# Optimization experiments

Hardware: AMD Instinct MI355X
Metric: run time of the kernel (lower is better)

The kernel has to match this reference:

```python
import jax, jax.numpy as jnp
import numpy as np

N = 20000      # nodes
E = 320000     # edges
B = 128        # graphs in batch
DIN = 64       # in_channels == out_channels (residual)
DEDGE = 64     # edge_attr_dim
DINS = 64      # ins_dim
H = 2          # heads
C = 64         # out_channels per head
L = 2          # num_ins (conv layers)
SLOPE = 0.2    # leaky relu negative slope
EPS = 1e-5     # batchnorm eps


def setup_inputs() -> dict:
    key = jax.random.key(0)
    ks = jax.random.split(key, 12)
    s = 0.05  # small glorot-ish init scale
    return {
        "x": jax.random.normal(ks[0], (N, DIN), jnp.float32),
        "edge_index": jax.random.randint(ks[1], (2, E), 0, N),
        "edge_attr": jax.random.normal(ks[2], (E, DEDGE), jnp.float32),
        "instr_vectors": jax.random.normal(ks[3], (L, B, DINS), jnp.float32),
        "batch": jnp.sort(jax.random.randint(ks[4], (N,), 0, B)),
        "W_l": jax.random.normal(ks[5], (L, DIN + DINS, H * C), jnp.float32) * s,
        "W_e": jax.random.normal(ks[6], (L, DEDGE + DINS, H * C), jnp.float32) * s,
        "att_l": jax.random.normal(ks[7], (L, H, C), jnp.float32) * s,
        "att_r": jax.random.normal(ks[8], (L, H, C), jnp.float32) * s,
        "att_e": jax.random.normal(ks[9], (L, H, C), jnp.float32) * s,
        "bias": jnp.zeros((L, C), jnp.float32),
        "bn_gamma": jnp.ones((L - 1, C), jnp.float32),
        "bn_beta": jnp.zeros((L - 1, C), jnp.float32),
    }


def reference(x, edge_index, edge_attr, instr_vectors, batch,
              W_l, W_e, att_l, att_r, att_e, bias, bn_gamma, bn_beta):
    src, dst = edge_index[0], edge_index[1]  # j -> i (source_to_target)
    h = x
    for i in range(L):
        ins = instr_vectors[i]                                   # [B, DINS]
        x_cat = jnp.concatenate([h, ins[batch]], axis=-1)        # [N, DIN+DINS]
        e_cat = jnp.concatenate([edge_attr, ins[batch[src]]], axis=-1)  # [E, ...]
        xl = (x_cat @ W_l[i]).reshape(-1, H, C)                  # [N,H,C] (lin_l == lin_r)
        al = (xl * att_l[i]).sum(-1)                             # [N,H]
        ar = (xl * att_r[i]).sum(-1)                             # [N,H]
        eh = (e_cat @ W_e[i]).reshape(-1, H, C)                  # [E,H,C]
        ae = (eh * att_e[i]).sum(-1)                             # [E,H]
        a = al[src] + ar[dst] + ae                               # [E,H]
        a = jnp.where(a > 0, a, SLOPE * a)                       # leaky relu
        # segment softmax over incoming edges of each target node
        m = jax.ops.segment_max(a, dst, num_segments=N)          # [N,H]
        ex = jnp.exp(a - m[dst])
        ssum = jax.ops.segment_sum(ex, dst, num_segments=N)
        alpha = ex / (ssum[dst] + 1e-16)                         # [E,H]
        out = jax.ops.segment_sum(xl[src] * alpha[:, :, None], dst, num_segments=N)
        out = out.mean(axis=1) + bias[i]                         # concat=False -> head mean
        h = out + h                                              # residual
        if i != L - 1:
            mu = h.mean(axis=0)
            var = ((h - mu) ** 2).mean(axis=0)                   # biased var (BN training)
            h = (h - mu) / jnp.sqrt(var + EPS) * bn_gamma[i] + bn_beta[i]
            h = jax.nn.relu(h)
    return h
```

## Files before the change

kernel.cpp:

```cpp
#include <hip/hip_runtime.h>
#include <hip/hip_fp16.h>
#include <math.h>

#define NN 20000
#define NE 320000
#define NB 128
#define SLOPE 0.2f
#define BN_EPS 1e-5f
#define NBLK 79
#define ROWS 65

__device__ __forceinline__ unsigned short f2bf(float f) {
    unsigned int u = __float_as_uint(f);
    unsigned int r = (u + 0x7FFFu + ((u >> 16) & 1u)) >> 16;
    return (unsigned short)r;
}
__device__ __forceinline__ float bf2f(unsigned short h) {
    return __uint_as_float(((unsigned int)h) << 16);
}

__global__ __launch_bounds__(256) void k_hist(const int* __restrict__ dst, int* __restrict__ deg) {
    int e = blockIdx.x * 256 + threadIdx.x;
    if (e < NE) atomicAdd(&deg[dst[e]], 1);
}

__global__ __launch_bounds__(256) void k_scanA(const int* __restrict__ deg, int* __restrict__ bsum) {
    __shared__ int wsum[4];
    int t = threadIdx.x;
    int idx = blockIdx.x * 256 + t;
    int v = (idx < NN) ? deg[idx] : 0;
    for (int off = 32; off > 0; off >>= 1) v += __shfl_xor(v, off);
    if ((t & 63) == 0) wsum[t >> 6] = v;
    __syncthreads();
    if (t == 0) bsum[blockIdx.x] = wsum[0] + wsum[1] + wsum[2] + wsum[3];
}

__global__ __launch_bounds__(64) void k_scanB(const int* __restrict__ bsum, int* __restrict__ boff,
                                              int* __restrict__ rowptr) {
    int l = threadIdx.x;
    int v0 = (l < NBLK) ? bsum[l] : 0;
    int v1 = (64 + l < NBLK) ? bsum[64 + l] : 0;
    int o0 = v0, o1 = v1;
    for (int off = 1; off < 64; off <<= 1) { int u = __shfl_up(v0, off); if (l >= off) v0 += u; }
    int tot0 = __shfl(v0, 63);
    for (int off = 1; off < 64; off <<= 1) { int u = __shfl_up(v1, off); if (l >= off) v1 += u; }
    int tot1 = __shfl(v1, 63);
    if (l < NBLK) boff[l] = v0 - o0;
    if (64 + l < NBLK) boff[64 + l] = tot0 + v1 - o1;
    if (l == 0) rowptr[NN] = tot0 + tot1;
}

__global__ __launch_bounds__(256) void k_scanC(const int* __restrict__ deg, const int* __restrict__ boff,
                                               int* __restrict__ rowptr, int* __restrict__ cursor) {
    __shared__ int wsum[4];
    int t = threadIdx.x, lane = t & 63, w = t >> 6;
    int idx = blockIdx.x * 256 + t;
    int v = (idx < NN) ? deg[idx] : 0;
    int incl = v;
    for (int off = 1; off < 64; off <<= 1) { int u = __shfl_up(incl, off); if (lane >= off) incl += u; }
    if (lane == 63) wsum[w] = incl;
    __syncthreads();
    int pre = 0;
    for (int i = 0; i < w; ++i) pre += wsum[i];
    int excl = incl - v + pre + boff[blockIdx.x];
    if (idx < NN) { rowptr[idx] = excl; cursor[idx] = excl; }
}

__global__ __launch_bounds__(256) void k_p1(const float* __restrict__ We, const float* __restrict__ atte,
                                            float* __restrict__ ve01, float* __restrict__ w2e01) {
    int L = blockIdx.x;
    const float* WeL = We + (size_t)L * 128 * 128;
    const float* aeL = atte + L * 128;
    int t = threadIdx.x;
    int h = (t >> 6) & 1;
    int k = t & 63;
    int row = (t < 128) ? k : (64 + k);
    float acc = 0.f;
    for (int c = 0; c < 64; ++c) acc += WeL[row * 128 + h * 64 + c] * aeL[h * 64 + c];
    if (t < 128) ve01[L * 128 + t] = acc;
    else        w2e01[L * 128 + (t - 128)] = acc;
}

__global__ __launch_bounds__(256) void k_p2both(const float* __restrict__ instr, const float* __restrict__ Wl,
                                                const float* __restrict__ w2e01,
                                                float* __restrict__ insl01, float* __restrict__ ce01) {
    int blk = blockIdx.x, t = threadIdx.x;
    if (blk < 128) {
        int L = blk >> 6;
        int idx = (blk & 63) * 256 + t;
        int b = idx >> 7, j = idx & 127;
        const float* ins = instr + (size_t)L * NB * 64;
        const float* WlL = Wl + (size_t)L * 128 * 128;
        float acc = 0.f;
        for (int k = 0; k < 64; ++k) acc += ins[b * 64 + k] * WlL[(64 + k) * 128 + j];
        insl01[(size_t)L * 16384 + idx] = acc;
    } else {
        int L = blk - 128;
        int b = t >> 1, h = t & 1;
        const float* ins = instr + (size_t)L * NB * 64;
        const float* w2 = w2e01 + L * 128 + h * 64;
        float acc = 0.f;
        for (int k = 0; k < 64; ++k) acc += ins[b * 64 + k] * w2[k];
        ce01[L * 256 + b * 2 + h] = acc;
    }
}

__global__ __launch_bounds__(256) void k_node(const float* __restrict__ hcur, const float* __restrict__ Wl,
                                              const float* __restrict__ insl, const int* __restrict__ batch,
                                              const float* __restrict__ attl, const float* __restrict__ attr_,
                                              const float2* __restrict__ ce2,
                                              const float* __restrict__ scsh, int use_bn,
                                              unsigned short* __restrict__ xlh,
                                              float* __restrict__ alc, float* __restrict__ ar) {
    __shared__ float sh[8 * 64];
    int t = threadIdx.x;
    int row0 = blockIdx.x * 8;
    for (int idx = t; idx < 512; idx += 256) {
        int r = idx >> 6, k = idx & 63;
        int n = row0 + r;
        float hv = (n < NN) ? hcur[n * 64 + k] : 0.f;
        if (use_bn) hv = fmaxf(hv * scsh[k] + scsh[64 + k], 0.f);
        sh[idx] = hv;
    }
    __syncthreads();
    int w = t >> 6, lane = t & 63;
    int h = w & 1;
    int rbase = (w >> 1) * 4;
    int j = h * 64 + lane;
    float attlv = attl[j];
    float attrv = attr_[j];
    float acc0 = 0.f, acc1 = 0.f, acc2 = 0.f, acc3 = 0.f;
    for (int k = 0; k < 64; ++k) {
        float wv = Wl[k * 128 + j];
        acc0 += sh[(rbase + 0) * 64 + k] * wv;
        acc1 += sh[(rbase + 1) * 64 + k] * wv;
        acc2 += sh[(rbase + 2) * 64 + k] * wv;
        acc3 += sh[(rbase + 3) * 64 + k] * wv;
    }
    float accs[4] = {acc0, acc1, acc2, acc3};
    for (int rr = 0; rr < 4; ++rr) {
        int n = row0 + rbase + rr;
        if (n >= NN) break;
        int b = batch[n];
        float v = accs[rr] + insl[b * 128 + j];
        xlh[(size_t)n * 128 + j] = f2bf(v);
        float pl = v * attlv, pr = v * attrv;
        for (int off = 32; off > 0; off >>= 1) {
            pl += __shfl_xor(pl, off);
            pr += __shfl_xor(pr, off);
        }
        if (lane == 0) {
            float2 cb = ce2[b];
            alc[n * 2 + h] = pl + (h ? cb.y : cb.x);
            ar[n * 2 + h] = pr;
        }
    }
}

__global__ __launch_bounds__(64) void k_sced(const int* __restrict__ src, const int* __restrict__ dst,
                                             const float* __restrict__ eattr, const float* __restrict__ ve01,
                                             const float2* __restrict__ alc2, const float2* __restrict__ ar2,
                                             int* __restrict__ cursor, int4* __restrict__ einfo) {
    __shared__ float se[64 * ROWS];
    __shared__ float svT[256];
    int lane = threadIdx.x;
#pragma unroll
    for (int i = 0; i < 4; ++i) {
        int idx = i * 64 + lane;
        svT[idx] = ve01[(idx & 3) * 64 + (idx >> 2)];
    }
    int ebase = blockIdx.x * 64;
    const float4* gsrc = (const float4*)eattr + (size_t)ebase * 16;
#pragma unroll
    for (int i = 0; i < 16; ++i) {
        int fi = i * 64 + lane;
        float4 f = gsrc[fi];
        int el = fi >> 4, q = fi & 15;
        float* dp = se + el * ROWS + q * 4;
        dp[0] = f.x; dp[1] = f.y; dp[2] = f.z; dp[3] = f.w;
    }
    const float* row = se + lane * ROWS;
    float d0 = 0.f, d1 = 0.f, d2 = 0.f, d3 = 0.f;
#pragma unroll
    for (int k = 0; k < 64; ++k) {
        float fv = row[k];
        float4 vt = *(const float4*)&svT[4 * k];
        d0 += fv * vt.x; d1 += fv * vt.y; d2 += fv * vt.z; d3 += fv * vt.w;
    }
    int e = ebase + lane;
    int s = src[e], dd = dst[e];
    float2 al = alc2[s], arr = ar2[dd];
    float a0 = al.x + arr.x + d0;
    float a1 = al.y + arr.y + d1;
    a0 = (a0 > 0.f) ? a0 : SLOPE * a0;
    a1 = (a1 > 0.f) ? a1 : SLOPE * a1;
    __half2 ex = __floats2half2_rn(__expf(a0), __expf(a1));
    __half2 d23 = __floats2half2_rn(d2, d3);
    int pos = atomicAdd(&cursor[dd], 1);
    einfo[pos] = make_int4(s | (dd << 15), *(int*)&d23, s, *(int*)&ex);
}

__global__ __launch_bounds__(256) void k_attnexp(const int4* __restrict__ einfo,
                                                 const float2* __restrict__ alc2, const float2* __restrict__ ar2,
                                                 int2* __restrict__ rec1) {
    int p = blockIdx.x * 256 + threadIdx.x;
    if (p >= NE) return;
    int4 r = einfo[p];
    int s = r.x & 0x7FFF, d = r.x >> 15;
    __half2 hd = *(__half2*)&r.y;
    float2 dv = __half22float2(hd);
    float2 a_l = alc2[s];
    float2 a_r = ar2[d];
    float a0 = a_l.x + a_r.x + dv.x;
    float a1 = a_l.y + a_r.y + dv.y;
    a0 = (a0 > 0.f) ? a0 : SLOPE * a0;
    a1 = (a1 > 0.f) ? a1 : SLOPE * a1;
    __half2 hx = __floats2half2_rn(__expf(a0), __expf(a1));
    rec1[p] = make_int2(s, *(int*)&hx);
}

__global__ __launch_bounds__(256) void k_gather(const int* __restrict__ rowptr, const int2* __restrict__ rec,
                                                int stride,
                                                const unsigned int* __restrict__ xl32,
                                                const float* __restrict__ bias, const float* __restrict__ hprev,
                                                const float* __restrict__ scsh, int use_bn,
                                                float* __restrict__ hnew) {
    int t = threadIdx.x;
    int w = t >> 6, lane = t & 63;
    int n = blockIdx.x * 4 + w;
    if (n >= NN) return;
    int r0 = rowptr[n], r1 = rowptr[n + 1];
    float acc0 = 0.f, acc1 = 0.f, ss = 0.f;
    const unsigned int* xlp = xl32 + lane;
#pragma unroll 8
    for (int p = r0; p < r1; ++p) {
        int2 r = rec[(size_t)p * stride];
        __half2 hx = *(__half2*)&r.y;
        float2 e2 = __half22float2(hx);
        float ex = (lane < 32) ? e2.x : e2.y;
        unsigned int pr = xlp[(size_t)r.x * 64];
        ss += ex;
        acc0 += ex * bf2f((unsigned short)(pr & 0xFFFFu));
        acc1 += ex * bf2f((unsigned short)(pr >> 16));
    }
    float inv_s = 1.f / (ss + 1e-16f);
    acc0 *= inv_s; acc1 *= inv_s;
    float o0 = 0.5f * (acc0 + __shfl_xor(acc0, 32));
    float o1 = 0.5f * (acc1 + __shfl_xor(acc1, 32));
    if (lane < 32) {
        float2 hv = ((const float2*)(hprev + (size_t)n * 64))[lane];
        if (use_bn) {
            float2 sc = ((const float2*)scsh)[lane];
            float2 sf = ((const float2*)(scsh + 64))[lane];
            hv.x = fmaxf(hv.x * sc.x + sf.x, 0.f);
            hv.y = fmaxf(hv.y * sc.y + sf.y, 0.f);
        }
        float2 bv = ((const float2*)bias)[lane];
        float2 o;
        o.x = o0 + bv.x + hv.x;
        o.y = o1 + bv.y + hv.y;
        ((float2*)(hnew + (size_t)n * 64))[lane] = o;
    }
}

__global__ __launch_bounds__(256) void k_bnstat(const float* __restrict__ hbuf,
                                                float* __restrict__ part, float* __restrict__ partsq) {
    __shared__ float sA[256], sB[256];
    int t = threadIdx.x;
    int c = t & 63, r = t >> 6;
    int n0 = blockIdx.x * 80;
    float s = 0.f, s2 = 0.f;
    for (int i = 0; i < 20; ++i) {
        float v = hbuf[(size_t)(n0 + i * 4 + r) * 64 + c];
        s += v; s2 += v * v;
    }
    sA[t] = s; sB[t] = s2;
    __syncthreads();
    if (t < 64) {
        part[blockIdx.x * 64 + t]   = sA[t] + sA[t + 64] + sA[t + 128] + sA[t + 192];
        partsq[blockIdx.x * 64 + t] = sB[t] + sB[t + 64] + sB[t + 128] + sB[t + 192];
    }
}

__global__ __launch_bounds__(256) void k_bnred(const float* __restrict__ part, const float* __restrict__ partsq,
                                               const float* __restrict__ gamma, const float* __restrict__ beta,
                                               float* __restrict__ scsh) {
    __shared__ float sA[256], sB[256];
    int t = threadIdx.x;
    int c = t & 63, q = t >> 6;
    float s = 0.f, s2 = 0.f;
    for (int j = q; j < 250; j += 4) { s += part[j * 64 + c]; s2 += partsq[j * 64 + c]; }
    sA[t] = s; sB[t] = s2;
    __syncthreads();
    if (t < 64) {
        float su = sA[t] + sA[t + 64] + sA[t + 128] + sA[t + 192];
        float sq = sB[t] + sB[t + 64] + sB[t + 128] + sB[t + 192];
        float mu = su * (1.f / NN);
        float var = sq * (1.f / NN) - mu * mu;
        float sc = gamma[t] * rsqrtf(var + BN_EPS);
        scsh[t] = sc;
        scsh[64 + t] = beta[t] - mu * sc;
    }
}

extern "C" void kernel_launch(void* const* d_in, const int* in_sizes, int n_in,
                              void* d_out, int out_size, void* d_ws, size_t ws_size,
                              hipStream_t stream) {
    (void)in_sizes; (void)n_in; (void)out_size; (void)ws_size;
    const float* x     = (const float*)d_in[0];
    const int*   eidx  = (const int*)d_in[1];
    const float* eattr = (const float*)d_in[2];
    const float* instr = (const float*)d_in[3];
    const int*   batch = (const int*)d_in[4];
    const float* W_l   = (const float*)d_in[5];
    const float* W_e   = (const float*)d_in[6];
    const float* att_l = (const float*)d_in[7];
    const float* att_r = (const float*)d_in[8];
    const float* att_e = (const float*)d_in[9];
    const float* bias  = (const float*)d_in[10];
    const float* bn_g  = (const float*)d_in[11];
    const float* bn_b  = (const float*)d_in[12];
    float* out = (float*)d_out;

    const int* src = eidx;
    const int* dst = eidx + NE;

    char* ws = (char*)d_ws;
    int4*   einfo   = (int4*)ws;       ws += (size_t)NE * 16;
    int2*   rec1    = (int2*)ws;       ws += (size_t)NE * 8;
    unsigned short* xlh = (unsigned short*)ws; ws += (size_t)NN * 128 * 2;
    int*    deg     = (int*)ws;        ws += NN * 4;
    int*    rowptr  = (int*)ws;        ws += (NN + 1) * 4 + 4;
    int*    cursor  = (int*)ws;        ws += NN * 4;
    int*    bsum    = (int*)ws;        ws += 80 * 4;
    int*    boff    = (int*)ws;        ws += 80 * 4;
    float*  alc     = (float*)ws;      ws += NN * 2 * 4;
    float*  ar      = (float*)ws;      ws += NN * 2 * 4;
    float*  insl01  = (float*)ws;      ws += 2 * 128 * 128 * 4;
    float*  ve01    = (float*)ws;      ws += 256 * 4;
    float*  w2e01   = (float*)ws;      ws += 256 * 4;
    float*  ce01    = (float*)ws;      ws += 2 * 256 * 4;
    float*  hbuf    = (float*)ws;      ws += (size_t)NN * 64 * 4;
    float*  part    = (float*)ws;      ws += 250 * 64 * 4;
    float*  partsq  = (float*)ws;      ws += 250 * 64 * 4;
    float*  scsh    = (float*)ws;      ws += 128 * 4;

    hipMemsetAsync(deg, 0, NN * 4, stream);
    k_hist<<<(NE + 255) / 256, 256, 0, stream>>>(dst, deg);
    k_scanA<<<NBLK, 256, 0, stream>>>(deg, bsum);
    k_scanB<<<1, 64, 0, stream>>>(bsum, boff, rowptr);
    k_scanC<<<NBLK, 256, 0, stream>>>(deg, boff, rowptr, cursor);

    k_p1<<<2, 256, 0, stream>>>(W_e, att_e, ve01, w2e01);
    k_p2both<<<130, 256, 0, stream>>>(instr, W_l, w2e01, insl01, ce01);

    k_node<<<(NN + 7) / 8, 256, 0, stream>>>(x, W_l, insl01, batch,
                                             att_l, att_r, (const float2*)ce01,
                                             scsh, 0, xlh, alc, ar);
    k_sced<<<NE / 64, 64, 0, stream>>>(src, dst, eattr, ve01,
                                       (const float2*)alc, (const float2*)ar, cursor, einfo);
    k_gather<<<NN / 4, 256, 0, stream>>>(rowptr, (const int2*)einfo + 1, 2,
                                         (const unsigned int*)xlh,
                                         bias, x, scsh, 0, hbuf);
    k_bnstat<<<250, 256, 0, stream>>>(hbuf, part, partsq);
    k_bnred<<<1, 256, 0, stream>>>(part, partsq, bn_g, bn_b, scsh);

    k_node<<<(NN + 7) / 8, 256, 0, stream>>>(hbuf, W_l + 128 * 128, insl01 + 16384, batch,
                                             att_l + 128, att_r + 128, (const float2*)(ce01 + 256),
                                             scsh, 1, xlh, alc, ar);
    k_attnexp<<<(NE + 255) / 256, 256, 0, stream>>>(einfo, (const float2*)alc, (const float2*)ar, rec1);
    k_gather<<<NN / 4, 256, 0, stream>>>(rowptr, rec1, 1, (const unsigned int*)xlh,
                                         bias + 64, hbuf, scsh, 1, out);
}
```

Measured before the change: 297.7 us.

## Fuse front-end kernels, single-block scan, BN stats into gather, attention into gather

```diff
diff --git a/kernel.cpp b/kernel.cpp
--- a/kernel.cpp
+++ b/kernel.cpp
@@ -7,7 +7,6 @@
 #define NB 128
 #define SLOPE 0.2f
 #define BN_EPS 1e-5f
-#define NBLK 79
 #define ROWS 65
 
 __device__ __forceinline__ unsigned short f2bf(float f) {
@@ -19,75 +18,20 @@
     return __uint_as_float(((unsigned int)h) << 16);
 }
 
-__global__ __launch_bounds__(256) void k_hist(const int* __restrict__ dst, int* __restrict__ deg) {
-    int e = blockIdx.x * 256 + threadIdx.x;
-    if (e < NE) atomicAdd(&deg[dst[e]], 1);
-}
-
-__global__ __launch_bounds__(256) void k_scanA(const int* __restrict__ deg, int* __restrict__ bsum) {
-    __shared__ int wsum[4];
-    int t = threadIdx.x;
-    int idx = blockIdx.x * 256 + t;
-    int v = (idx < NN) ? deg[idx] : 0;
-    for (int off = 32; off > 0; off >>= 1) v += __shfl_xor(v, off);
-    if ((t & 63) == 0) wsum[t >> 6] = v;
-    __syncthreads();
-    if (t == 0) bsum[blockIdx.x] = wsum[0] + wsum[1] + wsum[2] + wsum[3];
-}
-
-__global__ __launch_bounds__(64) void k_scanB(const int* __restrict__ bsum, int* __restrict__ boff,
-                                              int* __restrict__ rowptr) {
-    int l = threadIdx.x;
-    int v0 = (l < NBLK) ? bsum[l] : 0;
-    int v1 = (64 + l < NBLK) ? bsum[64 + l] : 0;
-    int o0 = v0, o1 = v1;
-    for (int off = 1; off < 64; off <<= 1) { int u = __shfl_up(v0, off); if (l >= off) v0 += u; }
-    int tot0 = __shfl(v0, 63);
-    for (int off = 1; off < 64; off <<= 1) { int u = __shfl_up(v1, off); if (l >= off) v1 += u; }
-    int tot1 = __shfl(v1, 63);
-    if (l < NBLK) boff[l] = v0 - o0;
-    if (64 + l < NBLK) boff[64 + l] = tot0 + v1 - o1;
-    if (l == 0) rowptr[NN] = tot0 + tot1;
-}
-
-__global__ __launch_bounds__(256) void k_scanC(const int* __restrict__ deg, const int* __restrict__ boff,
-                                               int* __restrict__ rowptr, int* __restrict__ cursor) {
-    __shared__ int wsum[4];
-    int t = threadIdx.x, lane = t & 63, w = t >> 6;
-    int idx = blockIdx.x * 256 + t;
-    int v = (idx < NN) ? deg[idx] : 0;
-    int incl = v;
-    for (int off = 1; off < 64; off <<= 1) { int u = __shfl_up(incl, off); if (lane >= off) incl += u; }
-    if (lane == 63) wsum[w] = incl;
-    __syncthreads();
-    int pre = 0;
-    for (int i = 0; i < w; ++i) pre += wsum[i];
-    int excl = incl - v + pre + boff[blockIdx.x];
-    if (idx < NN) { rowptr[idx] = excl; cursor[idx] = excl; }
-}
-
-__global__ __launch_bounds__(256) void k_p1(const float* __restrict__ We, const float* __restrict__ atte,
-                                            float* __restrict__ ve01, float* __restrict__ w2e01) {
-    int L = blockIdx.x;
-    const float* WeL = We + (size_t)L * 128 * 128;
-    const float* aeL = atte + L * 128;
-    int t = threadIdx.x;
-    int h = (t >> 6) & 1;
-    int k = t & 63;
-    int row = (t < 128) ? k : (64 + k);
-    float acc = 0.f;
-    for (int c = 0; c < 64; ++c) acc += WeL[row * 128 + h * 64 + c] * aeL[h * 64 + c];
-    if (t < 128) ve01[L * 128 + t] = acc;
-    else        w2e01[L * 128 + (t - 128)] = acc;
-}
-
-__global__ __launch_bounds__(256) void k_p2both(const float* __restrict__ instr, const float* __restrict__ Wl,
-                                                const float* __restrict__ w2e01,
-                                                float* __restrict__ insl01, float* __restrict__ ce01) {
+__global__ __launch_bounds__(256) void k_front(const int* __restrict__ dst, int* __restrict__ deg,
+                                               const float* __restrict__ instr, const float* __restrict__ Wl,
+                                               const float* __restrict__ We, const float* __restrict__ atte,
+                                               float* __restrict__ insl01, float* __restrict__ ve01,
+                                               float* __restrict__ ce01) {
+    __shared__ float w2[128];
     int blk = blockIdx.x, t = threadIdx.x;
-    if (blk < 128) {
-        int L = blk >> 6;
-        int idx = (blk & 63) * 256 + t;
+    if (blk < 1250) {
+        int e = blk * 256 + t;
+        atomicAdd(&deg[dst[e]], 1);
+    } else if (blk < 1378) {
+        int bb = blk - 1250;
+        int L = bb >> 6;
+        int idx = (bb & 63) * 256 + t;
         int b = idx >> 7, j = idx & 127;
         const float* ins = instr + (size_t)L * NB * 64;
         const float* WlL = Wl + (size_t)L * 128 * 128;
@@ -95,14 +39,45 @@
         for (int k = 0; k < 64; ++k) acc += ins[b * 64 + k] * WlL[(64 + k) * 128 + j];
         insl01[(size_t)L * 16384 + idx] = acc;
     } else {
-        int L = blk - 128;
-        int b = t >> 1, h = t & 1;
+        int L = blk - 1378;
+        const float* WeL = We + (size_t)L * 128 * 128;
+        const float* aeL = atte + L * 128;
+        int h = (t >> 6) & 1;
+        int k = t & 63;
+        int row = (t < 128) ? k : (64 + k);
+        float acc = 0.f;
+        for (int c = 0; c < 64; ++c) acc += WeL[row * 128 + h * 64 + c] * aeL[h * 64 + c];
+        if (t < 128) ve01[L * 128 + t] = acc;
+        else        w2[t - 128] = acc;
+        __syncthreads();
+        int b = t >> 1, hh = t & 1;
         const float* ins = instr + (size_t)L * NB * 64;
-        const float* w2 = w2e01 + L * 128 + h * 64;
-        float acc = 0.f;
-        for (int k = 0; k < 64; ++k) acc += ins[b * 64 + k] * w2[k];
-        ce01[L * 256 + b * 2 + h] = acc;
-    }
+        float a2 = 0.f;
+        for (int kk = 0; kk < 64; ++kk) a2 += ins[b * 64 + kk] * w2[hh * 64 + kk];
+        ce01[L * 256 + b * 2 + hh] = a2;
+    }
+}
+
+__global__ __launch_bounds__(1024) void k_scan(const int* __restrict__ deg,
+                                               int* __restrict__ rowptr, int* __restrict__ cursor) {
+    __shared__ int wsum[16];
+    int t = threadIdx.x, lane = t & 63, w = t >> 6;
+    int running = 0;
+    for (int r = 0; r < 20; ++r) {
+        int idx = r * 1024 + t;
+        int v = (idx < NN) ? deg[idx] : 0;
+        int incl = v;
+        for (int off = 1; off < 64; off <<= 1) { int u = __shfl_up(incl, off); if (lane >= off) incl += u; }
+        if (lane == 63) wsum[w] = incl;
+        __syncthreads();
+        int pre = 0, tot = 0;
+        for (int i = 0; i < 16; ++i) { int s = wsum[i]; tot += s; if (i < w) pre += s; }
+        int excl = running + pre + incl - v;
+        if (idx < NN) { rowptr[idx] = excl; cursor[idx] = excl; }
+        running += tot;
+        __syncthreads();
+    }
+    if (t == 0) rowptr[NN] = running;
 }
 
 __global__ __launch_bounds__(256) void k_node(const float* __restrict__ hcur, const float* __restrict__ Wl,
@@ -200,41 +175,25 @@
     einfo[pos] = make_int4(s | (dd << 15), *(int*)&d23, s, *(int*)&ex);
 }
 
-__global__ __launch_bounds__(256) void k_attnexp(const int4* __restrict__ einfo,
-                                                 const float2* __restrict__ alc2, const float2* __restrict__ ar2,
-                                                 int2* __restrict__ rec1) {
-    int p = blockIdx.x * 256 + threadIdx.x;
-    if (p >= NE) return;
-    int4 r = einfo[p];
-    int s = r.x & 0x7FFF, d = r.x >> 15;
-    __half2 hd = *(__half2*)&r.y;
-    float2 dv = __half22float2(hd);
-    float2 a_l = alc2[s];
-    float2 a_r = ar2[d];
-    float a0 = a_l.x + a_r.x + dv.x;
-    float a1 = a_l.y + a_r.y + dv.y;
-    a0 = (a0 > 0.f) ? a0 : SLOPE * a0;
-    a1 = (a1 > 0.f) ? a1 : SLOPE * a1;
-    __half2 hx = __floats2half2_rn(__expf(a0), __expf(a1));
-    rec1[p] = make_int2(s, *(int*)&hx);
-}
-
-__global__ __launch_bounds__(256) void k_gather(const int* __restrict__ rowptr, const int2* __restrict__ rec,
-                                                int stride,
-                                                const unsigned int* __restrict__ xl32,
-                                                const float* __restrict__ bias, const float* __restrict__ hprev,
-                                                const float* __restrict__ scsh, int use_bn,
-                                                float* __restrict__ hnew) {
+__global__ __launch_bounds__(256) void k_gather0(const int* __restrict__ rowptr, const int2* __restrict__ rec,
+                                                 const unsigned int* __restrict__ xl32,
+                                                 const float* __restrict__ bias, const float* __restrict__ hprev,
+                                                 float* __restrict__ hnew,
+                                                 float* __restrict__ part, int* __restrict__ ticket,
+                                                 const float* __restrict__ bn_g, const float* __restrict__ bn_b,
+                                                 float* __restrict__ scsh) {
+    __shared__ float smv[4][64];
+    __shared__ float smq[4][64];
+    __shared__ int lastflag;
     int t = threadIdx.x;
     int w = t >> 6, lane = t & 63;
     int n = blockIdx.x * 4 + w;
-    if (n >= NN) return;
     int r0 = rowptr[n], r1 = rowptr[n + 1];
     float acc0 = 0.f, acc1 = 0.f, ss = 0.f;
     const unsigned int* xlp = xl32 + lane;
 #pragma unroll 8
     for (int p = r0; p < r1; ++p) {
-        int2 r = rec[(size_t)p * stride];
+        int2 r = rec[(size_t)p * 2];
         __half2 hx = *(__half2*)&r.y;
         float2 e2 = __half22float2(hx);
         float ex = (lane < 32) ? e2.x : e2.y;
@@ -249,57 +208,85 @@
     float o1 = 0.5f * (acc1 + __shfl_xor(acc1, 32));
     if (lane < 32) {
         float2 hv = ((const float2*)(hprev + (size_t)n * 64))[lane];
-        if (use_bn) {
-            float2 sc = ((const float2*)scsh)[lane];
-            float2 sf = ((const float2*)(scsh + 64))[lane];
-            hv.x = fmaxf(hv.x * sc.x + sf.x, 0.f);
-            hv.y = fmaxf(hv.y * sc.y + sf.y, 0.f);
-        }
         float2 bv = ((const float2*)bias)[lane];
         float2 o;
         o.x = o0 + bv.x + hv.x;
         o.y = o1 + bv.y + hv.y;
         ((float2*)(hnew + (size_t)n * 64))[lane] = o;
-    }
-}
-
-__global__ __launch_bounds__(256) void k_bnstat(const float* __restrict__ hbuf,
-                                                float* __restrict__ part, float* __restrict__ partsq) {
-    __shared__ float sA[256], sB[256];
-    int t = threadIdx.x;
-    int c = t & 63, r = t >> 6;
-    int n0 = blockIdx.x * 80;
-    float s = 0.f, s2 = 0.f;
-    for (int i = 0; i < 20; ++i) {
-        float v = hbuf[(size_t)(n0 + i * 4 + r) * 64 + c];
-        s += v; s2 += v * v;
-    }
-    sA[t] = s; sB[t] = s2;
+        smv[w][2 * lane]     = o.x;
+        smv[w][2 * lane + 1] = o.y;
+        smq[w][2 * lane]     = o.x * o.x;
+        smq[w][2 * lane + 1] = o.y * o.y;
+    }
     __syncthreads();
-    if (t < 64) {
-        part[blockIdx.x * 64 + t]   = sA[t] + sA[t + 64] + sA[t + 128] + sA[t + 192];
-        partsq[blockIdx.x * 64 + t] = sB[t] + sB[t + 64] + sB[t + 128] + sB[t + 192];
-    }
-}
-
-__global__ __launch_bounds__(256) void k_bnred(const float* __restrict__ part, const float* __restrict__ partsq,
-                                               const float* __restrict__ gamma, const float* __restrict__ beta,
-                                               float* __restrict__ scsh) {
-    __shared__ float sA[256], sB[256];
-    int t = threadIdx.x;
-    int c = t & 63, q = t >> 6;
-    float s = 0.f, s2 = 0.f;
-    for (int j = q; j < 250; j += 4) { s += part[j * 64 + c]; s2 += partsq[j * 64 + c]; }
-    sA[t] = s; sB[t] = s2;
+    if (t < 128) {
+        int c = t & 63, which = t >> 6;
+        float a = which ? (smq[0][c] + smq[1][c] + smq[2][c] + smq[3][c])
+                        : (smv[0][c] + smv[1][c] + smv[2][c] + smv[3][c]);
+        atomicAdd(&part[(blockIdx.x & 63) * 128 + which * 64 + c], a);
+    }
+    __threadfence();
     __syncthreads();
-    if (t < 64) {
-        float su = sA[t] + sA[t + 64] + sA[t + 128] + sA[t + 192];
-        float sq = sB[t] + sB[t + 64] + sB[t + 128] + sB[t + 192];
+    if (t == 0) { int old = atomicAdd(ticket, 1); lastflag = (old == (NN / 4 - 1)); }
+    __syncthreads();
+    if (lastflag && t < 64) {
+        float su = 0.f, sq = 0.f;
+        for (int b = 0; b < 64; ++b) {
+            su += atomicAdd(&part[b * 128 + t], 0.f);
+            sq += atomicAdd(&part[b * 128 + 64 + t], 0.f);
+        }
         float mu = su * (1.f / NN);
         float var = sq * (1.f / NN) - mu * mu;
-        float sc = gamma[t] * rsqrtf(var + BN_EPS);
+        float sc = bn_g[t] * rsqrtf(var + BN_EPS);
         scsh[t] = sc;
-        scsh[64 + t] = beta[t] - mu * sc;
+        scsh[64 + t] = bn_b[t] - mu * sc;
+    }
+}
+
+__global__ __launch_bounds__(256) void k_gather1(const int* __restrict__ rowptr, const int4* __restrict__ einfo,
+                                                 const float2* __restrict__ alc2, const float2* __restrict__ ar2,
+                                                 const unsigned int* __restrict__ xl32,
+                                                 const float* __restrict__ bias, const float* __restrict__ hprev,
+                                                 const float* __restrict__ scsh, float* __restrict__ out) {
+    int t = threadIdx.x;
+    int w = t >> 6, lane = t & 63;
+    int n = blockIdx.x * 4 + w;
+    int r0 = rowptr[n], r1 = rowptr[n + 1];
+    float2 arr = ar2[n];
+    float acc0 = 0.f, acc1 = 0.f, ss = 0.f;
+    const unsigned int* xlp = xl32 + lane;
+#pragma unroll 4
+    for (int p = r0; p < r1; ++p) {
+        int4 r = einfo[p];
+        int s = r.z;
+        float2 dv = __half22float2(*(__half2*)&r.y);
+        float2 al = alc2[s];
+        float a0 = al.x + arr.x + dv.x;
+        float a1 = al.y + arr.y + dv.y;
+        a0 = (a0 > 0.f) ? a0 : SLOPE * a0;
+        a1 = (a1 > 0.f) ? a1 : SLOPE * a1;
+        float e0 = __expf(a0), e1 = __expf(a1);
+        float ex = (lane < 32) ? e0 : e1;
+        unsigned int pr = xlp[(size_t)s * 64];
+        ss += ex;
+        acc0 += ex * bf2f((unsigned short)(pr & 0xFFFFu));
+        acc1 += ex * bf2f((unsigned short)(pr >> 16));
+    }
+    float inv_s = 1.f / (ss + 1e-16f);
+    acc0 *= inv_s; acc1 *= inv_s;
+    float o0 = 0.5f * (acc0 + __shfl_xor(acc0, 32));
+    float o1 = 0.5f * (acc1 + __shfl_xor(acc1, 32));
+    if (lane < 32) {
+        float2 hv = ((const float2*)(hprev + (size_t)n * 64))[lane];
+        float2 sc = ((const float2*)scsh)[lane];
+        float2 sf = ((const float2*)(scsh + 64))[lane];
+        hv.x = fmaxf(hv.x * sc.x + sf.x, 0.f);
+        hv.y = fmaxf(hv.y * sc.y + sf.y, 0.f);
+        float2 bv = ((const float2*)bias)[lane];
+        float2 o;
+        o.x = o0 + bv.x + hv.x;
+        o.y = o1 + bv.y + hv.y;
+        ((float2*)(out + (size_t)n * 64))[lane] = o;
     }
 }
 
@@ -327,48 +314,35 @@
 
     char* ws = (char*)d_ws;
     int4*   einfo   = (int4*)ws;       ws += (size_t)NE * 16;
-    int2*   rec1    = (int2*)ws;       ws += (size_t)NE * 8;
     unsigned short* xlh = (unsigned short*)ws; ws += (size_t)NN * 128 * 2;
     int*    deg     = (int*)ws;        ws += NN * 4;
-    int*    rowptr  = (int*)ws;        ws += (NN + 1) * 4 + 4;
+    float*  part    = (float*)ws;      ws += 64 * 128 * 4;
+    int*    ticket  = (int*)ws;        ws += 16;
+    int*    rowptr  = (int*)ws;        ws += (NN + 1) * 4 + 12;
     int*    cursor  = (int*)ws;        ws += NN * 4;
-    int*    bsum    = (int*)ws;        ws += 80 * 4;
-    int*    boff    = (int*)ws;        ws += 80 * 4;
     float*  alc     = (float*)ws;      ws += NN * 2 * 4;
     float*  ar      = (float*)ws;      ws += NN * 2 * 4;
     float*  insl01  = (float*)ws;      ws += 2 * 128 * 128 * 4;
     float*  ve01    = (float*)ws;      ws += 256 * 4;
-    float*  w2e01   = (float*)ws;      ws += 256 * 4;
     float*  ce01    = (float*)ws;      ws += 2 * 256 * 4;
     float*  hbuf    = (float*)ws;      ws += (size_t)NN * 64 * 4;
-    float*  part    = (float*)ws;      ws += 250 * 64 * 4;
-    float*  partsq  = (float*)ws;      ws += 250 * 64 * 4;
     float*  scsh    = (float*)ws;      ws += 128 * 4;
 
-    hipMemsetAsync(deg, 0, NN * 4, stream);
-    k_hist<<<(NE + 255) / 256, 256, 0, stream>>>(dst, deg);
-    k_scanA<<<NBLK, 256, 0, stream>>>(deg, bsum);
-    k_scanB<<<1, 64, 0, stream>>>(bsum, boff, rowptr);
-    k_scanC<<<NBLK, 256, 0, stream>>>(deg, boff, rowptr, cursor);
-
-    k_p1<<<2, 256, 0, stream>>>(W_e, att_e, ve01, w2e01);
-    k_p2both<<<130, 256, 0, stream>>>(instr, W_l, w2e01, insl01, ce01);
-
+    hipMemsetAsync(deg, 0, NN * 4 + 64 * 128 * 4 + 16, stream);
+
+    k_front<<<1380, 256, 0, stream>>>(dst, deg, instr, W_l, W_e, att_e, insl01, ve01, ce01);
+    k_scan<<<1, 1024, 0, stream>>>(deg, rowptr, cursor);
     k_node<<<(NN + 7) / 8, 256, 0, stream>>>(x, W_l, insl01, batch,
                                              att_l, att_r, (const float2*)ce01,
                                              scsh, 0, xlh, alc, ar);
     k_sced<<<NE / 64, 64, 0, stream>>>(src, dst, eattr, ve01,
                                        (const float2*)alc, (const float2*)ar, cursor, einfo);
-    k_gather<<<NN / 4, 256, 0, stream>>>(rowptr, (const int2*)einfo + 1, 2,
-                                         (const unsigned int*)xlh,
-                                         bias, x, scsh, 0, hbuf);
-    k_bnstat<<<250, 256, 0, stream>>>(hbuf, part, partsq);
-    k_bnred<<<1, 256, 0, stream>>>(part, partsq, bn_g, bn_b, scsh);
-
+    k_gather0<<<NN / 4, 256, 0, stream>>>(rowptr, (const int2*)einfo + 1,
+                                          (const unsigned int*)xlh, bias, x, hbuf,
+                                          part, ticket, bn_g, bn_b, scsh);
     k_node<<<(NN + 7) / 8, 256, 0, stream>>>(hbuf, W_l + 128 * 128, insl01 + 16384, batch,
                                              att_l + 128, att_r + 128, (const float2*)(ce01 + 256),
                                              scsh, 1, xlh, alc, ar);
-    k_attnexp<<<(NE + 255) / 256, 256, 0, stream>>>(einfo, (const float2*)alc, (const float2*)ar, rec1);
-    k_gather<<<NN / 4, 256, 0, stream>>>(rowptr, rec1, 1, (const unsigned int*)xlh,
-                                         bias + 64, hbuf, scsh, 1, out);
-}
+    k_gather1<<<NN / 4, 256, 0, stream>>>(rowptr, einfo, (const float2*)alc, (const float2*)ar,
+                                          (const unsigned int*)xlh, bias + 64, hbuf, scsh, out);
+}
```

New measurement: 671.6 us. +125.6%, slower.
